# Kernel tuning notes

Measured on AMD Instinct MI355X. Metric: run time of the kernel, lower is better.

## Reference

```python
import jax, jax.numpy as jnp
import numpy as np

NUM_PTM_TYPES = 26
NUM_PER_TYPE = 128
TEMPERATURE = 0.07


def setup_inputs() -> dict:
    key = jax.random.key(0)
    k1, k2, k3 = jax.random.split(key, 3)
    N, D = 8192, 256
    x = jax.random.normal(k1, (N, D), dtype=jnp.float32)
    Q = jax.random.randint(k2, (N,), 0, NUM_PTM_TYPES)
    E = jax.random.normal(k3, (NUM_PTM_TYPES * NUM_PER_TYPE, D), dtype=jnp.float32)
    E = E / jnp.linalg.norm(E, axis=1, keepdims=True)  # matches _initialize_embeddings
    return {"x": x, "Q": Q, "E": E, "tau": 1}


def _quantize_grouped(x, Q, E, tau):
    # Vectorized form of the per-PTM-type loop: every type owns an equal-size
    # sub-codebook of NUM_PER_TYPE rows, so gather each token's sub-codebook.
    D = x.shape[-1]
    cb = E.reshape(NUM_PTM_TYPES, NUM_PER_TYPE, D)[Q]          # [N, K, D]
    dot = jnp.einsum('nd,nkd->nk', x, cb) / tau                # [N, K]
    sim = jax.nn.softmax(dot, axis=-1)
    z_q = jnp.einsum('nk,nkd->nd', sim, cb)                    # [N, D]
    idx = jnp.argmax(sim, axis=-1) + Q * NUM_PER_TYPE          # global code index
    return z_q, idx


def _uniform_loss(E):
    K = E.shape[0]
    En = E / jnp.linalg.norm(E, axis=1, keepdims=True)
    sim = En @ En.T                                            # [K, K]
    labels = jnp.arange(K) // NUM_PER_TYPE
    labels_eq = labels[None, :] == labels[:, None]
    eye = jnp.eye(K, dtype=bool)
    sim = jnp.where(eye, -jnp.inf, sim)
    sim_exp = jnp.exp(sim / TEMPERATURE)                       # diagonal -> 0
    sum_exp = jnp.sum(sim_exp, axis=1)
    pos_sum_exp = jnp.sum(sim_exp * labels_eq.astype(sim_exp.dtype), axis=1)
    return -jnp.mean(jnp.log(pos_sum_exp / sum_exp))


def reference(x, Q, E, tau):
    tau = jnp.float32(tau)
    quantized, encoding_indices = _quantize_grouped(x, Q, E, tau)
    loss = jnp.float32(0.0)
    uniform_loss = _uniform_loss(E)
    return quantized, loss, uniform_loss, encoding_indices
```

## Files before the change

### kernel.cpp

```cpp
#include <hip/hip_runtime.h>
#include <hip/hip_bf16.h>

#define NUM_TYPES 26
#define NPT 128
#define DIMS 256
#define K_TOTAL 3328
#define N_TOK 8192
#define INV_TEMP (1.0f/0.07f)
#define TM 32
#define MAX_TILES 16
#define NHIST 32

typedef unsigned short ushort_t;
typedef short bf16x8 __attribute__((ext_vector_type(8)));
typedef float f32x4 __attribute__((ext_vector_type(4)));

__device__ __forceinline__ float wave_reduce_sum(float v){
#pragma unroll
  for (int off = 32; off; off >>= 1) v += __shfl_xor(v, off);
  return v;
}

__device__ __forceinline__ unsigned short f2bf(float f){
  __hip_bfloat16 h = __float2bfloat16(f);
  return __builtin_bit_cast(unsigned short, h);
}

#define GLOAD_LDS16(g, s) \
  __builtin_amdgcn_global_load_lds((__attribute__((address_space(1))) void*)(g), \
                                   (__attribute__((address_space(3))) void*)(s), 16, 0, 0)

#define VMWAIT(N) do{ asm volatile("s_waitcnt vmcnt(" #N ")" ::: "memory"); \
                      __builtin_amdgcn_sched_barrier(0); }while(0)

__global__ __launch_bounds__(256) void prepk(const float* __restrict__ E,
                                             const int* __restrict__ Q,
                                             ushort_t* __restrict__ Enb,
                                             float* __restrict__ EA,
                                             ushort_t* __restrict__ EC,
                                             int* __restrict__ bh){
  const int t = threadIdx.x;
  const int b = blockIdx.x;
  if (b < 832){
    const int w = t >> 6, l = t & 63;
    const int row = b * 4 + w;
    float4 v = reinterpret_cast<const float4*>(E + (size_t)row * DIMS)[l];
    float ss = v.x*v.x + v.y*v.y + v.z*v.z + v.w*v.w;
    ss = wave_reduce_sum(ss);
    const float inv = 1.0f / sqrtf(ss);
    ushort4 o;
    o.x = f2bf(v.x * inv); o.y = f2bf(v.y * inv);
    o.z = f2bf(v.z * inv); o.w = f2bf(v.w * inv);
    reinterpret_cast<ushort4*>(Enb + (size_t)row * DIMS)[l] = o;
    return;
  }
  if (b < 936){
    const int id = b - 832;
    const int tp = id >> 2, ck = id & 3;
    __shared__ float T[32][260];
    const int row = t >> 3, sub = t & 7;
    const float* src = E + (size_t)(tp*NPT + ck*32 + row) * DIMS;
#pragma unroll
    for (int i = 0; i < 8; ++i){
      const int c4 = sub + 8*i;
      *(f32x4*)(&T[row][c4*4]) = *(const f32x4*)(src + c4*4);
    }
    __syncthreads();
    ushort_t* dst = EC + (size_t)(tp*4 + ck) * 8192;
#pragma unroll
    for (int i = 0; i < 4; ++i){
      const int si = t + i*256;
      const int sec = si >> 8, d = (si >> 2) & 63, s = si & 3;
      const int cb8 = (s ^ ((d >> 1) & 3)) * 8;
      union { bf16x8 v8; ushort_t u[8]; } pk;
#pragma unroll
      for (int j = 0; j < 8; ++j)
        pk.u[j] = f2bf(T[cb8 + j][sec*64 + d]);
      *(bf16x8*)(dst + (size_t)si*8) = pk.v8;
    }
    return;
  }
  if (b < 1144){
    const int id = b - 936;
    const int tp = id >> 3, kt = id & 7;
    float* dst = EA + (size_t)(tp*8 + kt) * 4096;
    const float* src = E + (size_t)tp * NPT * DIMS;
#pragma unroll
    for (int i = 0; i < 16; ++i){
      const int e = i*256 + t;
      const int sec = e >> 10, code = (e >> 3) & 127, hp = (e >> 2) & 1, j = e & 3;
      const int dim = sec*64 + kt*8 + (hp ^ ((code >> 2) & 1))*4 + j;
      dst[e] = src[(size_t)code*DIMS + dim];
    }
    return;
  }
  {
    __shared__ int h[NUM_TYPES];
    if (t < NUM_TYPES) h[t] = 0;
    __syncthreads();
    const int c = b - 1144;
    atomicAdd(&h[Q[c*256 + t]], 1);
    __syncthreads();
    if (t < NUM_TYPES) bh[c*NUM_TYPES + t] = h[t];
  }
}

__global__ __launch_bounds__(256) void gramk(const ushort_t* __restrict__ Enb,
                                             const int* __restrict__ Q,
                                             const int* __restrict__ bh,
                                             int* __restrict__ counts,
                                             int* __restrict__ offsets,
                                             int* __restrict__ perm,
                                             float* __restrict__ part){
  const int bi = blockIdx.y, bj = blockIdx.x;
  const int t = threadIdx.x;
  if (bi > bj){
    const int lid = bi*(bi-1)/2 + bj;
    if (lid >= NHIST) return;
    __shared__ int sh_tot[NUM_TYPES], sh_off[NUM_TYPES], sh_cur[NUM_TYPES];
    if (t < NUM_TYPES){
      int s = 0;
      for (int h = 0; h < NHIST; ++h) s += bh[h*NUM_TYPES + t];
      sh_tot[t] = s;
    }
    __syncthreads();
    if (t == 0){
      int s = 0;
      for (int g = 0; g < NUM_TYPES; ++g){ sh_off[g] = s; s += sh_tot[g]; }
    }
    __syncthreads();
    if (t < NUM_TYPES){
      int run = sh_off[t];
      for (int h = 0; h < lid; ++h) run += bh[h*NUM_TYPES + t];
      sh_cur[t] = run;
      if (lid == 0){ counts[t] = sh_tot[t]; offsets[t] = sh_off[t]; }
    }
    __syncthreads();
    const int i = lid*256 + t;
    const int q = Q[i];
    const int pos = atomicAdd(&sh_cur[q], 1);
    perm[pos] = i;
    return;
  }
  __shared__ ushort_t As[128*64];
  __shared__ ushort_t Bs[128*64];
  __shared__ float rs[128][2];
  __shared__ float cs[128][2];
  const int w = t >> 6, l = t & 63;
  const int wr = w >> 1, wc = w & 1;
  const int lrow = l & 15;
  const int lk = (l >> 4) * 8;
  const int hi = l >> 4;

  f32x4 acc[4][4];
#pragma unroll
  for (int m = 0; m < 4; ++m)
#pragma unroll
    for (int n = 0; n < 4; ++n) acc[m][n] = (f32x4){0.f, 0.f, 0.f, 0.f};

  for (int kt = 0; kt < 4; ++kt){
    if (kt) __syncthreads();
#pragma unroll
    for (int p = 0; p < 4; ++p){
      const int cbase = p*256 + w*64;
      const int c = cbase + l;
      const int row = c >> 3;
      const int kcol = (c & 7) * 8;
      const ushort_t* gA = Enb + (size_t)(bi*128 + row) * DIMS + kt*64 + kcol;
      const ushort_t* gB = Enb + (size_t)(bj*128 + row) * DIMS + kt*64 + kcol;
      GLOAD_LDS16(gA, As + (size_t)cbase*8);
      GLOAD_LDS16(gB, Bs + (size_t)cbase*8);
    }
    __syncthreads();
#pragma unroll
    for (int kk = 0; kk < 2; ++kk){
      bf16x8 a[4], b[4];
#pragma unroll
      for (int m = 0; m < 4; ++m)
        a[m] = *reinterpret_cast<const bf16x8*>(&As[(wr*64 + m*16 + lrow)*64 + kk*32 + lk]);
#pragma unroll
      for (int n = 0; n < 4; ++n)
        b[n] = *reinterpret_cast<const bf16x8*>(&Bs[(wc*64 + n*16 + lrow)*64 + kk*32 + lk]);
#pragma unroll
      for (int m = 0; m < 4; ++m)
#pragma unroll
        for (int n = 0; n < 4; ++n)
          acc[m][n] = __builtin_amdgcn_mfma_f32_16x16x32_bf16(a[m], b[n], acc[m][n], 0, 0, 0);
    }
  }

#pragma unroll
  for (int m = 0; m < 4; ++m)
#pragma unroll
    for (int n = 0; n < 4; ++n)
#pragma unroll
      for (int j = 0; j < 4; ++j){
        const int grow = bi*128 + wr*64 + m*16 + hi*4 + j;
        const int gcol = bj*128 + wc*64 + n*16 + lrow;
        const float g = acc[m][n][j];
        acc[m][n][j] = (grow == gcol) ? 0.f : __expf(g * INV_TEMP);
      }

#pragma unroll
  for (int m = 0; m < 4; ++m)
#pragma unroll
    for (int j = 0; j < 4; ++j){
      float s = 0.f;
#pragma unroll
      for (int n = 0; n < 4; ++n) s += acc[m][n][j];
#pragma unroll
      for (int off = 1; off < 16; off <<= 1) s += __shfl_xor(s, off);
      if (lrow == 0) rs[wr*64 + m*16 + hi*4 + j][wc] = s;
    }
  if (bi != bj){
#pragma unroll
    for (int n = 0; n < 4; ++n){
      float c = 0.f;
#pragma unroll
      for (int m = 0; m < 4; ++m)
#pragma unroll
        for (int j = 0; j < 4; ++j) c += acc[m][n][j];
      c += __shfl_xor(c, 16); c += __shfl_xor(c, 32);
      if (hi == 0) cs[wc*64 + n*16 + lrow][wr] = c;
    }
  }
  __syncthreads();
  if (t < 128){
    part[(size_t)bj*K_TOTAL + bi*128 + t] = rs[t][0] + rs[t][1];
    if (bi != bj)
      part[(size_t)bi*K_TOTAL + bj*128 + t] = cs[t][0] + cs[t][1];
  }
}

__device__ __forceinline__ void stageA5(const float* EA, char* dst, int tp, int kt,
                                        int sec, int cg, int l){
  const char* src = (const char*)(EA + (size_t)(tp*8 + kt) * 4096) + sec*4096 + cg*2048;
  char* d = dst + sec*4096 + cg*2048;
#pragma unroll
  for (int i = 0; i < 2; ++i)
    GLOAD_LDS16(src + i*1024 + l*16, d + i*1024);
}

__device__ __forceinline__ void stageC5(const ushort_t* EC, char* dst, int tp, int ck,
                                        int sec, int dh, int l){
  const char* src = (const char*)(EC + (size_t)(tp*4 + ck) * 8192) + sec*4096 + dh*2048;
  char* d = dst + sec*4096 + dh*2048;
#pragma unroll
  for (int i = 0; i < 2; ++i)
    GLOAD_LDS16(src + i*1024 + l*16, d + i*1024);
}

__global__ __launch_bounds__(512, 1) void quantg(const float* __restrict__ x,
                                                 const float* __restrict__ EA,
                                                 const ushort_t* __restrict__ EC,
                                                 const float* __restrict__ part,
                                                 const int* __restrict__ counts,
                                                 const int* __restrict__ offsets,
                                                 const int* __restrict__ perm,
                                                 const int* __restrict__ taup,
                                                 float* __restrict__ outZ,
                                                 float* __restrict__ outMisc,
                                                 float* __restrict__ outIdx){
  const int t = threadIdx.x;
  const int tp = blockIdx.x, rb = blockIdx.y;
  __shared__ __align__(16) char arena[81920];

  if (tp == NUM_TYPES){
    if (rb) return;
    float acc = 0.f;
    for (int i = t; i < K_TOTAL; i += 512){
      float s = 0.f;
#pragma unroll
      for (int bb = 0; bb < NUM_TYPES; ++bb) s += part[(size_t)bb*K_TOTAL + i];
      acc += logf(s) - logf(part[(size_t)(i >> 7)*K_TOTAL + i]);
    }
    acc = wave_reduce_sum(acc);
    float* red = (float*)arena;
    if ((t & 63) == 0) red[t >> 6] = acc;
    __syncthreads();
    if (t == 0){
      float s = 0.f;
#pragma unroll
      for (int i2 = 0; i2 < 8; ++i2) s += red[i2];
      outMisc[0] = 0.f; outMisc[1] = s / (float)K_TOTAL;
    }
    return;
  }

  const int cnt = counts[tp];
  if (rb * TM >= cnt) return;
  const int nt = min(TM, cnt - rb * TM);
  const int off = offsets[tp] + rb * TM;

  char* XA = arena;
  char* BA = arena + 32768;
  char* PB = arena;
  char* SB = arena + 67840;
  char* BC = arena;

  const int w = t >> 6, l = t & 63;
  const int sec = w >> 1;
  const int cg  = w & 1;
  const int tx = l & 15, ty = l >> 4;

  const int ti = *taup;
  const float tau = (ti > 0 && ti < (1 << 23)) ? (float)ti : __int_as_float(ti);
  const float inv_tau = 1.0f / tau;

#pragma unroll
  for (int i = 0; i < 4; ++i){
    const int row = w*4 + i;
    const int tid = (row < nt) ? perm[off + row] : perm[off];
    const int sc = (l & 56) | ((l & 7) ^ (row & 7));
    GLOAD_LDS16(x + (size_t)tid*DIMS + sc*4, XA + row*1024);
  }
  stageA5(EA, BA,         tp, 0, sec, cg, l);
  stageA5(EA, BA + 16384, tp, 1, sec, cg, l);
  __syncthreads();

  float acc[8][4];
#pragma unroll
  for (int rr = 0; rr < 8; ++rr)
#pragma unroll
    for (int cc = 0; cc < 4; ++cc) acc[rr][cc] = 0.f;

#pragma unroll
  for (int kt = 0; kt < 8; ++kt){
    if (kt < 6) stageA5(EA, BA + ((kt+2)%3)*16384, tp, kt+2, sec, cg, l);
    if (kt >= 2){
      if (kt < 6)      { VMWAIT(4); }
      else if (kt == 6){ VMWAIT(2); }
      else             { VMWAIT(0); }
    }
    const char* bbuf = BA + (kt%3)*16384 + sec*4096 + cg*2048;
#pragma unroll
    for (int q = 0; q < 2; ++q){
      f32x4 a[8], b[4];
#pragma unroll
      for (int rr = 0; rr < 8; ++rr){
        const int row = rr*4 + ty;
        const int c = (sec*16 + kt*2 + q) ^ (row & 7);
        a[rr] = *(const f32x4*)(XA + row*1024 + c*16);
      }
#pragma unroll
      for (int cc = 0; cc < 4; ++cc){
        const int codeg = tx + 16*cc;
        const int code  = cg*64 + codeg;
        const int slot = q ^ ((code >> 2) & 1);
        b[cc] = *(const f32x4*)(bbuf + codeg*32 + slot*16);
      }
#pragma unroll
      for (int rr = 0; rr < 8; ++rr)
#pragma unroll
        for (int cc = 0; cc < 4; ++cc)
#pragma unroll
          for (int e = 0; e < 4; ++e)
            acc[rr][cc] = fmaf(a[rr][e], b[cc][e], acc[rr][cc]);
    }
  }
  __syncthreads();

#pragma unroll
  for (int rr = 0; rr < 8; ++rr){
    const int row = rr*4 + ty;
#pragma unroll
    for (int cc = 0; cc < 4; ++cc)
      *(float*)(PB + sec*16896 + row*528 + (cg*64 + tx + 16*cc)*4) = acc[rr][cc];
  }
  __syncthreads();

  {
    const int r = t >> 4, s = t & 15;
    f32x4 v0 = (f32x4){0,0,0,0}, v1 = (f32x4){0,0,0,0};
#pragma unroll
    for (int ww = 0; ww < 4; ++ww){
      v0 += *(const f32x4*)(PB + ww*16896 + r*528 + s*32);
      v1 += *(const f32x4*)(PB + ww*16896 + r*528 + s*32 + 16);
    }
    float v[8];
#pragma unroll
    for (int e = 0; e < 4; ++e){ v[e] = v0[e]*inv_tau; v[4+e] = v1[e]*inv_tau; }
    float m = v[0]; int mi = s*8;
#pragma unroll
    for (int j = 1; j < 8; ++j) if (v[j] > m){ m = v[j]; mi = s*8 + j; }
#pragma unroll
    for (int o = 1; o < 16; o <<= 1){
      const float om = __shfl_xor(m, o);
      const int   oi = __shfl_xor(mi, o);
      if (om > m || (om == m && oi < mi)){ m = om; mi = oi; }
    }
    float e8[8]; float sum = 0.f;
#pragma unroll
    for (int j = 0; j < 8; ++j){ e8[j] = __expf(v[j] - m); sum += e8[j]; }
#pragma unroll
    for (int o = 1; o < 16; o <<= 1) sum += __shfl_xor(sum, o);
    const float inv = 1.0f / sum;
    union { bf16x8 v8; ushort_t u[8]; } pk;
#pragma unroll
    for (int j = 0; j < 8; ++j) pk.u[j] = f2bf(e8[j] * inv);
    *(bf16x8*)(SB + r*272 + s*16) = pk.v8;
    if (s == 0 && r < nt)
      outIdx[perm[off + r]] = (float)(mi + tp * NPT);
  }
  __syncthreads();

  stageC5(EC, BC,         tp, 0, sec, cg, l);
  stageC5(EC, BC + 16384, tp, 1, sec, cg, l);
  f32x4 zacc[2][2];
#pragma unroll
  for (int g = 0; g < 2; ++g)
#pragma unroll
    for (int n = 0; n < 2; ++n) zacc[g][n] = (f32x4){0,0,0,0};
#pragma unroll
  for (int ck = 0; ck < 4; ++ck){
    if (ck < 2) stageC5(EC, BC + ((ck+2)%3)*16384, tp, ck+2, sec, cg, l);
    if (ck < 2)      { VMWAIT(4); }
    else if (ck == 2){ VMWAIT(2); }
    else             { VMWAIT(0); }
    const char* bbuf = BC + (ck%3)*16384 + sec*4096 + cg*2048;
#pragma unroll
    for (int g = 0; g < 2; ++g){
      const bf16x8 af = *(const bf16x8*)(SB + (g*16 + tx)*272 + ck*64 + ty*16);
#pragma unroll
      for (int n = 0; n < 2; ++n){
        const int dsec = cg*32 + n*16 + tx;
        const int slot = ty ^ ((dsec >> 1) & 3);
        const bf16x8 bf = *(const bf16x8*)(bbuf + (n*16 + tx)*64 + slot*16);
        zacc[g][n] = __builtin_amdgcn_mfma_f32_16x16x32_bf16(af, bf, zacc[g][n], 0, 0, 0);
      }
    }
  }
#pragma unroll
  for (int g = 0; g < 2; ++g)
#pragma unroll
    for (int n = 0; n < 2; ++n)
#pragma unroll
      for (int j = 0; j < 4; ++j){
        const int row = g*16 + ty*4 + j;
        if (row < nt)
          outZ[(size_t)perm[off + row]*DIMS + sec*64 + cg*32 + n*16 + tx] = zacc[g][n][j];
      }
}

extern "C" void kernel_launch(void* const* d_in, const int* in_sizes, int n_in,
                              void* d_out, int out_size, void* d_ws, size_t ws_size,
                              hipStream_t stream){
  const float* x  = (const float*)d_in[0];
  const int*   Q  = (const int*)d_in[1];
  const float* E  = (const float*)d_in[2];
  const int* taup = (const int*)d_in[3];

  float* outZ    = (float*)d_out;
  float* outMisc = outZ + (size_t)N_TOK * DIMS;
  float* outIdx  = outMisc + 2;

  char* wsp = (char*)d_ws;
  ushort_t* Enb = (ushort_t*)wsp;
  float* part   = (float*)(wsp + 1703936);
  float* EA     = (float*)(wsp + 2050048);
  ushort_t* EC  = (ushort_t*)(wsp + 5457920);
  int* bh       = (int*)(wsp + 7161856);
  int* counts   = (int*)(wsp + 7165184);
  int* offsets  = (int*)(wsp + 7165312);
  int* perm     = (int*)(wsp + 7165440);

  prepk<<<1176, 256, 0, stream>>>(E, Q, Enb, EA, EC, bh);
  gramk<<<dim3(26, 26), 256, 0, stream>>>(Enb, Q, bh, counts, offsets, perm, part);
  quantg<<<dim3(NUM_TYPES + 1, MAX_TILES), 512, 0, stream>>>(x, EA, EC, part,
                                                             counts, offsets, perm,
                                                             taup, outZ, outMisc, outIdx);
}
```

Measured before the change: 47.85 us.

## Halve token tile and compute logits directly from global memory without LDS staging

Shrinks the per-block token tile from 32 to 16 rows and doubles the tile grid, so twice as many blocks run per type. The logit stage no longer stages x and the codebook through LDS with a pipelined async copy. Each thread now owns one code and reads its codebook slice from a new contiguous layout, reading x rows directly from global memory (likely cached broadcasts). This cuts LDS use and adds parallelism, at the cost of more redundant global and cache reads of x and less reuse per block.

```diff
diff --git a/kernel.cpp b/kernel.cpp
--- a/kernel.cpp
+++ b/kernel.cpp
@@ -7,8 +7,8 @@
 #define K_TOTAL 3328
 #define N_TOK 8192
 #define INV_TEMP (1.0f/0.07f)
-#define TM 32
-#define MAX_TILES 16
+#define TM 16
+#define MAX_TILES 32
 #define NHIST 32
 
 typedef unsigned short ushort_t;
@@ -36,7 +36,7 @@
 __global__ __launch_bounds__(256) void prepk(const float* __restrict__ E,
                                              const int* __restrict__ Q,
                                              ushort_t* __restrict__ Enb,
-                                             float* __restrict__ EA,
+                                             float* __restrict__ EA2,
                                              ushort_t* __restrict__ EC,
                                              int* __restrict__ bh){
   const int t = threadIdx.x;
@@ -83,14 +83,13 @@
   if (b < 1144){
     const int id = b - 936;
     const int tp = id >> 3, kt = id & 7;
-    float* dst = EA + (size_t)(tp*8 + kt) * 4096;
+    float* dst = EA2 + (size_t)tp*32768 + kt*1024;
     const float* src = E + (size_t)tp * NPT * DIMS;
 #pragma unroll
     for (int i = 0; i < 16; ++i){
       const int e = i*256 + t;
-      const int sec = e >> 10, code = (e >> 3) & 127, hp = (e >> 2) & 1, j = e & 3;
-      const int dim = sec*64 + kt*8 + (hp ^ ((code >> 2) & 1))*4 + j;
-      dst[e] = src[(size_t)code*DIMS + dim];
+      const int sec = e >> 10, code = (e >> 3) & 127, j = e & 7;
+      dst[sec*8192 + code*8 + j] = src[(size_t)code*DIMS + sec*64 + kt*8 + j];
     }
     return;
   }
@@ -232,15 +231,6 @@
   }
 }
 
-__device__ __forceinline__ void stageA5(const float* EA, char* dst, int tp, int kt,
-                                        int sec, int cg, int l){
-  const char* src = (const char*)(EA + (size_t)(tp*8 + kt) * 4096) + sec*4096 + cg*2048;
-  char* d = dst + sec*4096 + cg*2048;
-#pragma unroll
-  for (int i = 0; i < 2; ++i)
-    GLOAD_LDS16(src + i*1024 + l*16, d + i*1024);
-}
-
 __device__ __forceinline__ void stageC5(const ushort_t* EC, char* dst, int tp, int ck,
                                         int sec, int dh, int l){
   const char* src = (const char*)(EC + (size_t)(tp*4 + ck) * 8192) + sec*4096 + dh*2048;
@@ -251,7 +241,7 @@
 }
 
 __global__ __launch_bounds__(512, 1) void quantg(const float* __restrict__ x,
-                                                 const float* __restrict__ EA,
+                                                 const float* __restrict__ EA2,
                                                  const ushort_t* __restrict__ EC,
                                                  const float* __restrict__ part,
                                                  const int* __restrict__ counts,
@@ -263,7 +253,7 @@
                                                  float* __restrict__ outIdx){
   const int t = threadIdx.x;
   const int tp = blockIdx.x, rb = blockIdx.y;
-  __shared__ __align__(16) char arena[81920];
+  __shared__ __align__(16) char arena[53504];
 
   if (tp == NUM_TYPES){
     if (rb) return;
@@ -292,11 +282,9 @@
   const int nt = min(TM, cnt - rb * TM);
   const int off = offsets[tp] + rb * TM;
 
-  char* XA = arena;
-  char* BA = arena + 32768;
   char* PB = arena;
-  char* SB = arena + 67840;
   char* BC = arena;
+  char* SB = arena + 49152;
 
   const int w = t >> 6, l = t & 63;
   const int sec = w >> 1;
@@ -307,75 +295,44 @@
   const float tau = (ti > 0 && ti < (1 << 23)) ? (float)ti : __int_as_float(ti);
   const float inv_tau = 1.0f / tau;
 
-#pragma unroll
-  for (int i = 0; i < 4; ++i){
-    const int row = w*4 + i;
-    const int tid = (row < nt) ? perm[off + row] : perm[off];
-    const int sc = (l & 56) | ((l & 7) ^ (row & 7));
-    GLOAD_LDS16(x + (size_t)tid*DIMS + sc*4, XA + row*1024);
-  }
-  stageA5(EA, BA,         tp, 0, sec, cg, l);
-  stageA5(EA, BA + 16384, tp, 1, sec, cg, l);
+  int tid16[16];
+#pragma unroll
+  for (int rr = 0; rr < 16; ++rr)
+    tid16[rr] = (rr < nt) ? perm[off + rr] : perm[off];
+
+  float acc[16];
+#pragma unroll
+  for (int rr = 0; rr < 16; ++rr) acc[rr] = 0.f;
+
+  const int code = cg*64 + l;
+  const float* ea = EA2 + (size_t)tp*32768 + sec*8192 + code*8;
+#pragma unroll
+  for (int kt = 0; kt < 8; ++kt){
+    const f32x4 b0 = *(const f32x4*)(ea + kt*1024);
+    const f32x4 b1 = *(const f32x4*)(ea + kt*1024 + 4);
+#pragma unroll
+    for (int rr = 0; rr < 16; ++rr){
+      const float* xr = x + (size_t)tid16[rr]*DIMS + sec*64 + kt*8;
+#pragma unroll
+      for (int e = 0; e < 4; ++e){
+        acc[rr] = fmaf(xr[e],     b0[e], acc[rr]);
+        acc[rr] = fmaf(xr[4 + e], b1[e], acc[rr]);
+      }
+    }
+  }
+
+#pragma unroll
+  for (int rr = 0; rr < 16; ++rr)
+    *(float*)(PB + sec*8192 + rr*512 + code*4) = acc[rr];
   __syncthreads();
 
-  float acc[8][4];
-#pragma unroll
-  for (int rr = 0; rr < 8; ++rr)
-#pragma unroll
-    for (int cc = 0; cc < 4; ++cc) acc[rr][cc] = 0.f;
-
-#pragma unroll
-  for (int kt = 0; kt < 8; ++kt){
-    if (kt < 6) stageA5(EA, BA + ((kt+2)%3)*16384, tp, kt+2, sec, cg, l);
-    if (kt >= 2){
-      if (kt < 6)      { VMWAIT(4); }
-      else if (kt == 6){ VMWAIT(2); }
-      else             { VMWAIT(0); }
-    }
-    const char* bbuf = BA + (kt%3)*16384 + sec*4096 + cg*2048;
-#pragma unroll
-    for (int q = 0; q < 2; ++q){
-      f32x4 a[8], b[4];
-#pragma unroll
-      for (int rr = 0; rr < 8; ++rr){
-        const int row = rr*4 + ty;
-        const int c = (sec*16 + kt*2 + q) ^ (row & 7);
-        a[rr] = *(const f32x4*)(XA + row*1024 + c*16);
-      }
-#pragma unroll
-      for (int cc = 0; cc < 4; ++cc){
-        const int codeg = tx + 16*cc;
-        const int code  = cg*64 + codeg;
-        const int slot = q ^ ((code >> 2) & 1);
-        b[cc] = *(const f32x4*)(bbuf + codeg*32 + slot*16);
-      }
-#pragma unroll
-      for (int rr = 0; rr < 8; ++rr)
-#pragma unroll
-        for (int cc = 0; cc < 4; ++cc)
-#pragma unroll
-          for (int e = 0; e < 4; ++e)
-            acc[rr][cc] = fmaf(a[rr][e], b[cc][e], acc[rr][cc]);
-    }
-  }
-  __syncthreads();
-
-#pragma unroll
-  for (int rr = 0; rr < 8; ++rr){
-    const int row = rr*4 + ty;
-#pragma unroll
-    for (int cc = 0; cc < 4; ++cc)
-      *(float*)(PB + sec*16896 + row*528 + (cg*64 + tx + 16*cc)*4) = acc[rr][cc];
-  }
-  __syncthreads();
-
-  {
+  if (t < 256){
     const int r = t >> 4, s = t & 15;
     f32x4 v0 = (f32x4){0,0,0,0}, v1 = (f32x4){0,0,0,0};
 #pragma unroll
     for (int ww = 0; ww < 4; ++ww){
-      v0 += *(const f32x4*)(PB + ww*16896 + r*528 + s*32);
-      v1 += *(const f32x4*)(PB + ww*16896 + r*528 + s*32 + 16);
+      v0 += *(const f32x4*)(PB + ww*8192 + r*512 + s*32);
+      v1 += *(const f32x4*)(PB + ww*8192 + r*512 + s*32 + 16);
     }
     float v[8];
 #pragma unroll
@@ -406,11 +363,9 @@
 
   stageC5(EC, BC,         tp, 0, sec, cg, l);
   stageC5(EC, BC + 16384, tp, 1, sec, cg, l);
-  f32x4 zacc[2][2];
-#pragma unroll
-  for (int g = 0; g < 2; ++g)
-#pragma unroll
-    for (int n = 0; n < 2; ++n) zacc[g][n] = (f32x4){0,0,0,0};
+  f32x4 zacc[2];
+#pragma unroll
+  for (int n = 0; n < 2; ++n) zacc[n] = (f32x4){0,0,0,0};
 #pragma unroll
   for (int ck = 0; ck < 4; ++ck){
     if (ck < 2) stageC5(EC, BC + ((ck+2)%3)*16384, tp, ck+2, sec, cg, l);
@@ -418,28 +373,23 @@
     else if (ck == 2){ VMWAIT(2); }
     else             { VMWAIT(0); }
     const char* bbuf = BC + (ck%3)*16384 + sec*4096 + cg*2048;
-#pragma unroll
-    for (int g = 0; g < 2; ++g){
-      const bf16x8 af = *(const bf16x8*)(SB + (g*16 + tx)*272 + ck*64 + ty*16);
-#pragma unroll
-      for (int n = 0; n < 2; ++n){
-        const int dsec = cg*32 + n*16 + tx;
-        const int slot = ty ^ ((dsec >> 1) & 3);
-        const bf16x8 bf = *(const bf16x8*)(bbuf + (n*16 + tx)*64 + slot*16);
-        zacc[g][n] = __builtin_amdgcn_mfma_f32_16x16x32_bf16(af, bf, zacc[g][n], 0, 0, 0);
-      }
-    }
-  }
-#pragma unroll
-  for (int g = 0; g < 2; ++g)
-#pragma unroll
-    for (int n = 0; n < 2; ++n)
-#pragma unroll
-      for (int j = 0; j < 4; ++j){
-        const int row = g*16 + ty*4 + j;
-        if (row < nt)
-          outZ[(size_t)perm[off + row]*DIMS + sec*64 + cg*32 + n*16 + tx] = zacc[g][n][j];
-      }
+    const bf16x8 af = *(const bf16x8*)(SB + tx*272 + ck*64 + ty*16);
+#pragma unroll
+    for (int n = 0; n < 2; ++n){
+      const int dsec = cg*32 + n*16 + tx;
+      const int slot = ty ^ ((dsec >> 1) & 3);
+      const bf16x8 bf = *(const bf16x8*)(bbuf + (n*16 + tx)*64 + slot*16);
+      zacc[n] = __builtin_amdgcn_mfma_f32_16x16x32_bf16(af, bf, zacc[n], 0, 0, 0);
+    }
+  }
+#pragma unroll
+  for (int n = 0; n < 2; ++n)
+#pragma unroll
+    for (int j = 0; j < 4; ++j){
+      const int row = ty*4 + j;
+      if (row < nt)
+        outZ[(size_t)perm[off + row]*DIMS + sec*64 + cg*32 + n*16 + tx] = zacc[n][j];
+    }
 }
 
 extern "C" void kernel_launch(void* const* d_in, const int* in_sizes, int n_in,
@@ -457,16 +407,16 @@
   char* wsp = (char*)d_ws;
   ushort_t* Enb = (ushort_t*)wsp;
   float* part   = (float*)(wsp + 1703936);
-  float* EA     = (float*)(wsp + 2050048);
+  float* EA2    = (float*)(wsp + 2050048);
   ushort_t* EC  = (ushort_t*)(wsp + 5457920);
   int* bh       = (int*)(wsp + 7161856);
   int* counts   = (int*)(wsp + 7165184);
   int* offsets  = (int*)(wsp + 7165312);
   int* perm     = (int*)(wsp + 7165440);
 
-  prepk<<<1176, 256, 0, stream>>>(E, Q, Enb, EA, EC, bh);
+  prepk<<<1176, 256, 0, stream>>>(E, Q, Enb, EA2, EC, bh);
   gramk<<<dim3(26, 26), 256, 0, stream>>>(Enb, Q, bh, counts, offsets, perm, part);
-  quantg<<<dim3(NUM_TYPES + 1, MAX_TILES), 512, 0, stream>>>(x, EA, EC, part,
+  quantg<<<dim3(NUM_TYPES + 1, MAX_TILES), 512, 0, stream>>>(x, EA2, EC, part,
                                                              counts, offsets, perm,
                                                              taup, outZ, outMisc, outIdx);
 }
```

Result: slower. 95.90 us (+100.4%).

## Load codebook tiles directly from global into registers instead of LDS staging

Applied to the files above, without the earlier changes.

The dot-product phase of quantg no longer stages codebook tiles through a triple-buffered LDS pipeline. Each thread now reads its 8-float code slices straight from a relaid-out global buffer (EA2), which prepk writes in a contiguous per-code layout. The grid is also transposed so that blocks sharing a PTM type are adjacent, improving L2 reuse of that type's codebook. This removes LDS traffic and vmcnt waits and shrinks shared memory, but exposes global-load latency without explicit prefetch and duplicates reads across the row-direction waves.

```diff
diff --git a/kernel.cpp b/kernel.cpp
--- a/kernel.cpp
+++ b/kernel.cpp
@@ -36,7 +36,7 @@
 __global__ __launch_bounds__(256) void prepk(const float* __restrict__ E,
                                              const int* __restrict__ Q,
                                              ushort_t* __restrict__ Enb,
-                                             float* __restrict__ EA,
+                                             float* __restrict__ EA2,
                                              ushort_t* __restrict__ EC,
                                              int* __restrict__ bh){
   const int t = threadIdx.x;
@@ -83,14 +83,13 @@
   if (b < 1144){
     const int id = b - 936;
     const int tp = id >> 3, kt = id & 7;
-    float* dst = EA + (size_t)(tp*8 + kt) * 4096;
+    float* dst = EA2 + (size_t)tp*32768 + kt*1024;
     const float* src = E + (size_t)tp * NPT * DIMS;
 #pragma unroll
     for (int i = 0; i < 16; ++i){
       const int e = i*256 + t;
-      const int sec = e >> 10, code = (e >> 3) & 127, hp = (e >> 2) & 1, j = e & 3;
-      const int dim = sec*64 + kt*8 + (hp ^ ((code >> 2) & 1))*4 + j;
-      dst[e] = src[(size_t)code*DIMS + dim];
+      const int sec = e >> 10, code = (e >> 3) & 127, j = e & 7;
+      dst[sec*8192 + code*8 + j] = src[(size_t)code*DIMS + sec*64 + kt*8 + j];
     }
     return;
   }
@@ -232,15 +231,6 @@
   }
 }
 
-__device__ __forceinline__ void stageA5(const float* EA, char* dst, int tp, int kt,
-                                        int sec, int cg, int l){
-  const char* src = (const char*)(EA + (size_t)(tp*8 + kt) * 4096) + sec*4096 + cg*2048;
-  char* d = dst + sec*4096 + cg*2048;
-#pragma unroll
-  for (int i = 0; i < 2; ++i)
-    GLOAD_LDS16(src + i*1024 + l*16, d + i*1024);
-}
-
 __device__ __forceinline__ void stageC5(const ushort_t* EC, char* dst, int tp, int ck,
                                         int sec, int dh, int l){
   const char* src = (const char*)(EC + (size_t)(tp*4 + ck) * 8192) + sec*4096 + dh*2048;
@@ -251,7 +241,7 @@
 }
 
 __global__ __launch_bounds__(512, 1) void quantg(const float* __restrict__ x,
-                                                 const float* __restrict__ EA,
+                                                 const float* __restrict__ EA2,
                                                  const ushort_t* __restrict__ EC,
                                                  const float* __restrict__ part,
                                                  const int* __restrict__ counts,
@@ -262,8 +252,8 @@
                                                  float* __restrict__ outMisc,
                                                  float* __restrict__ outIdx){
   const int t = threadIdx.x;
-  const int tp = blockIdx.x, rb = blockIdx.y;
-  __shared__ __align__(16) char arena[81920];
+  const int rb = blockIdx.x, tp = blockIdx.y;
+  __shared__ __align__(16) char arena[72192];
 
   if (tp == NUM_TYPES){
     if (rb) return;
@@ -293,10 +283,9 @@
   const int off = offsets[tp] + rb * TM;
 
   char* XA = arena;
-  char* BA = arena + 32768;
   char* PB = arena;
+  char* BC = arena;
   char* SB = arena + 67840;
-  char* BC = arena;
 
   const int w = t >> 6, l = t & 63;
   const int sec = w >> 1;
@@ -314,8 +303,6 @@
     const int sc = (l & 56) | ((l & 7) ^ (row & 7));
     GLOAD_LDS16(x + (size_t)tid*DIMS + sc*4, XA + row*1024);
   }
-  stageA5(EA, BA,         tp, 0, sec, cg, l);
-  stageA5(EA, BA + 16384, tp, 1, sec, cg, l);
   __syncthreads();
 
   float acc[8][4];
@@ -324,18 +311,19 @@
 #pragma unroll
     for (int cc = 0; cc < 4; ++cc) acc[rr][cc] = 0.f;
 
+  const float* ea = EA2 + (size_t)tp*32768 + sec*8192;
 #pragma unroll
   for (int kt = 0; kt < 8; ++kt){
-    if (kt < 6) stageA5(EA, BA + ((kt+2)%3)*16384, tp, kt+2, sec, cg, l);
-    if (kt >= 2){
-      if (kt < 6)      { VMWAIT(4); }
-      else if (kt == 6){ VMWAIT(2); }
-      else             { VMWAIT(0); }
-    }
-    const char* bbuf = BA + (kt%3)*16384 + sec*4096 + cg*2048;
+    f32x4 b0[4], b1[4];
+#pragma unroll
+    for (int cc = 0; cc < 4; ++cc){
+      const float* p = ea + kt*1024 + (size_t)(cg*64 + tx + 16*cc)*8;
+      b0[cc] = *(const f32x4*)(p);
+      b1[cc] = *(const f32x4*)(p + 4);
+    }
 #pragma unroll
     for (int q = 0; q < 2; ++q){
-      f32x4 a[8], b[4];
+      f32x4 a[8];
 #pragma unroll
       for (int rr = 0; rr < 8; ++rr){
         const int row = rr*4 + ty;
@@ -343,19 +331,12 @@
         a[rr] = *(const f32x4*)(XA + row*1024 + c*16);
       }
 #pragma unroll
-      for (int cc = 0; cc < 4; ++cc){
-        const int codeg = tx + 16*cc;
-        const int code  = cg*64 + codeg;
-        const int slot = q ^ ((code >> 2) & 1);
-        b[cc] = *(const f32x4*)(bbuf + codeg*32 + slot*16);
-      }
-#pragma unroll
       for (int rr = 0; rr < 8; ++rr)
 #pragma unroll
         for (int cc = 0; cc < 4; ++cc)
 #pragma unroll
           for (int e = 0; e < 4; ++e)
-            acc[rr][cc] = fmaf(a[rr][e], b[cc][e], acc[rr][cc]);
+            acc[rr][cc] = fmaf(a[rr][e], (q ? b1 : b0)[cc][e], acc[rr][cc]);
     }
   }
   __syncthreads();
@@ -457,16 +438,16 @@
   char* wsp = (char*)d_ws;
   ushort_t* Enb = (ushort_t*)wsp;
   float* part   = (float*)(wsp + 1703936);
-  float* EA     = (float*)(wsp + 2050048);
+  float* EA2    = (float*)(wsp + 2050048);
   ushort_t* EC  = (ushort_t*)(wsp + 5457920);
   int* bh       = (int*)(wsp + 7161856);
   int* counts   = (int*)(wsp + 7165184);
   int* offsets  = (int*)(wsp + 7165312);
   int* perm     = (int*)(wsp + 7165440);
 
-  prepk<<<1176, 256, 0, stream>>>(E, Q, Enb, EA, EC, bh);
+  prepk<<<1176, 256, 0, stream>>>(E, Q, Enb, EA2, EC, bh);
   gramk<<<dim3(26, 26), 256, 0, stream>>>(Enb, Q, bh, counts, offsets, perm, part);
-  quantg<<<dim3(NUM_TYPES + 1, MAX_TILES), 512, 0, stream>>>(x, EA, EC, part,
+  quantg<<<dim3(MAX_TILES, NUM_TYPES + 1), 512, 0, stream>>>(x, EA2, EC, part,
                                                              counts, offsets, perm,
                                                              taup, outZ, outMisc, outIdx);
 }
```

Result: no change. 47.88 us (+0.1%).
